# Optimization experiments

Measured on AMD Instinct MI355X. Metric: run time of the kernel, lower is better.

The kernel has to match this reference:

```python
import jax, jax.numpy as jnp
import numpy as np

N_NODES = 50000
N_EDGES = 800000
N_GRAPHS = 64
FEAT, EMB, HID, VOCAB = 128, 256, 512, 512


def setup_inputs() -> dict:
    key = jax.random.key(0)
    ks = jax.random.split(key, 16)
    def w(k, shape, fan_in):
        return jax.random.normal(k, shape, jnp.float32) / np.sqrt(fan_in)
    return {
        "prev_symbol": jax.random.randint(ks[0], (N_GRAPHS,), 0, VOCAB, jnp.int32),
        "x": jax.random.normal(ks[1], (N_NODES, FEAT), jnp.float32),
        "edge_index": jax.random.randint(ks[2], (2, N_EDGES), 0, N_NODES, jnp.int64),
        "batch": jnp.sort(jax.random.randint(ks[3], (N_NODES,), 0, N_GRAPHS, jnp.int64)),
        "W_root1": w(ks[4], (FEAT, EMB), FEAT),
        "W_rel1": w(ks[5], (FEAT, EMB), FEAT),
        "b1": jnp.zeros((EMB,), jnp.float32),
        "W_root2": w(ks[6], (EMB, HID), EMB),
        "W_rel2": w(ks[7], (EMB, HID), EMB),
        "b2": jnp.zeros((HID,), jnp.float32),
        "Wh": w(ks[8], (HID, HID), HID),
        "bh": jnp.zeros((HID,), jnp.float32),
        "Wc": w(ks[9], (HID, HID), HID),
        "bc": jnp.zeros((HID,), jnp.float32),
        "Wout": w(ks[10], (HID, VOCAB), HID),
        "bout": jnp.zeros((VOCAB,), jnp.float32),
    }


def _rgcn(x, edge_index, W_root, W_rel, b):
    # single-relation RGCNConv: root transform + mean-aggregated neighbor messages
    src, dst = edge_index[0], edge_index[1]
    msg = x[src] @ W_rel                                   # [E, out]
    agg = jax.ops.segment_sum(msg, dst, num_segments=N_NODES)
    cnt = jax.ops.segment_sum(jnp.ones((src.shape[0],), x.dtype), dst,
                              num_segments=N_NODES)
    agg = agg / jnp.maximum(cnt, 1.0)[:, None]
    return x @ W_root + agg + b


def reference(prev_symbol, x, edge_index, batch,
              W_root1, W_rel1, b1, W_root2, W_rel2, b2,
              Wh, bh, Wc, bc, Wout, bout):
    h = jax.nn.relu(_rgcn(x, edge_index, W_root1, W_rel1, b1))
    h = jax.nn.relu(_rgcn(h, edge_index, W_root2, W_rel2, b2))
    # global_mean_pool over graph ids
    s = jax.ops.segment_sum(h, batch, num_segments=N_GRAPHS)
    n = jax.ops.segment_sum(jnp.ones((h.shape[0],), h.dtype), batch,
                            num_segments=N_GRAPHS)
    pooled = s / jnp.maximum(n, 1.0)[:, None]              # [G, HID]
    hidden = pooled @ Wh + bh
    cell = pooled @ Wc + bc
    logits = jax.nn.log_softmax(hidden @ Wout + bout, axis=1)
    return (logits, hidden, cell)
```

## Files before the change

### kernel.cpp

```cpp
#include <hip/hip_runtime.h>
#include <hip/hip_bf16.h>

#define N_NODES 50000
#define N_EDGES 800000
#define N_GRAPHS 64
#define FEAT 128
#define EMB 256
#define HID 512
#define VOCAB 512

#define RB ((N_NODES + 127) / 128)
#define RPX ((RB + 7) / 8)
#define EPT 8
#define EPB (256 * EPT)
#define FILL_BLOCKS ((N_EDGES + EPB - 1) / EPB)
#define BKT 64
#define CONV_ELEMS (N_NODES * 32 + 256 * 256 + 512 * 512)
#define CONV_BLOCKS (CONV_ELEMS / 256)

typedef __attribute__((ext_vector_type(4))) float floatx4;
typedef __attribute__((ext_vector_type(2))) float floatx2;
typedef unsigned int uint32;
typedef unsigned char uchar_t;

__device__ __forceinline__ void accf8(uint32 u, float* a) {
    floatx2 lo = __builtin_amdgcn_cvt_pk_f32_fp8(u, false);
    floatx2 hi = __builtin_amdgcn_cvt_pk_f32_fp8(u, true);
    a[0] += lo[0]; a[1] += lo[1]; a[2] += hi[0]; a[3] += hi[1];
}
__device__ __forceinline__ uchar_t f2f8(float v) {
    return (uchar_t)(__builtin_amdgcn_cvt_pk_fp8_f32(v, v, 0, false) & 0xff);
}
__device__ __forceinline__ uint32 pk4f8(float a, float b, float c, float d) {
    uint32 w = __builtin_amdgcn_cvt_pk_fp8_f32(a, b, 0, false);
    return __builtin_amdgcn_cvt_pk_fp8_f32(c, d, w, true);
}
__device__ __forceinline__ void async16(const void* g, void* l) {
    __builtin_amdgcn_global_load_lds(
        (const __attribute__((address_space(1))) void*)g,
        (__attribute__((address_space(3))) void*)l, 16, 0, 0);
}

__global__ void prep_kernel(const int* __restrict__ edge, int* __restrict__ cursor,
                            int* __restrict__ srcbuf,
                            const float* __restrict__ x,
                            const float* __restrict__ W01, const float* __restrict__ W11,
                            const float* __restrict__ W02, const float* __restrict__ W12,
                            uchar_t* __restrict__ xa8,
                            uchar_t* __restrict__ w1t8, uchar_t* __restrict__ w2t8) {
    if (blockIdx.x < FILL_BLOCKS) {
        int base = blockIdx.x * EPB + threadIdx.x;
        #pragma unroll
        for (int i = 0; i < EPT; ++i) {
            int e = base + i * 256;
            if (e < N_EDGES) {
                int dst = edge[N_EDGES + e];
                int src = edge[e];
                int pos = atomicAdd(cursor + dst, 1);
                if (pos < BKT) srcbuf[(dst << 6) + pos] = src;
            }
        }
    } else {
        int tid = (blockIdx.x - FILL_BLOCKS) * 256 + threadIdx.x;
        if (tid < N_NODES * 32) {
            int row = tid >> 5, c = (tid & 31) * 4;
            float4 v = *(const float4*)(x + (size_t)row * FEAT + c);
            *(uint32*)(xa8 + (size_t)row * 256 + c) = pk4f8(v.x, v.y, v.z, v.w);
        } else if (tid < N_NODES * 32 + 256 * 256) {
            int t1 = tid - N_NODES * 32;
            int n = t1 >> 8, k = t1 & 255;
            float v = (k < 128) ? W01[(size_t)k * 256 + n] : W11[(size_t)(k - 128) * 256 + n];
            w1t8[t1] = f2f8(v);
        } else {
            int t2 = tid - N_NODES * 32 - 256 * 256;
            int n = t2 >> 9, k = t2 & 511;
            float v = (k < 256) ? W02[(size_t)k * 512 + n] : W12[(size_t)(k - 256) * 512 + n];
            w2t8[t2] = f2f8(v);
        }
    }
}

__global__ __launch_bounds__(256) void gather1_kernel(
    const int* __restrict__ cursor, const int* __restrict__ srcbuf,
    uchar_t* __restrict__ xa8)
{
    int node = blockIdx.x * 4 + (threadIdx.x >> 6);
    if (node >= N_NODES) return;
    int lane = threadIdx.x & 63;
    int grp = lane >> 3;
    int l8 = lane & 7;
    int cnt = cursor[node];
    float ri = 1.0f / (float)max(cnt, 1);
    int beg = node << 6;
    int end = beg + min(cnt, BKT);

    float a[16];
    #pragma unroll
    for (int k = 0; k < 16; ++k) a[k] = 0.f;

    int j = beg + grp;
    for (; j + 8 < end; j += 16) {
        int s0 = srcbuf[j];
        int s1 = srcbuf[j + 8];
        uint4 u0 = *(const uint4*)(xa8 + (size_t)s0 * 256 + l8 * 16);
        uint4 u1 = *(const uint4*)(xa8 + (size_t)s1 * 256 + l8 * 16);
        accf8(u0.x, a + 0); accf8(u0.y, a + 4); accf8(u0.z, a + 8); accf8(u0.w, a + 12);
        accf8(u1.x, a + 0); accf8(u1.y, a + 4); accf8(u1.z, a + 8); accf8(u1.w, a + 12);
    }
    for (; j < end; j += 8) {
        int s0 = srcbuf[j];
        uint4 u0 = *(const uint4*)(xa8 + (size_t)s0 * 256 + l8 * 16);
        accf8(u0.x, a + 0); accf8(u0.y, a + 4); accf8(u0.z, a + 8); accf8(u0.w, a + 12);
    }
    #pragma unroll
    for (int k = 0; k < 16; ++k) a[k] += __shfl_down(a[k], 32);
    #pragma unroll
    for (int k = 0; k < 16; ++k) a[k] += __shfl_down(a[k], 16);
    #pragma unroll
    for (int k = 0; k < 16; ++k) a[k] += __shfl_down(a[k], 8);
    if (grp == 0) {
        uint4 o;
        o.x = pk4f8(a[0] * ri,  a[1] * ri,  a[2] * ri,  a[3] * ri);
        o.y = pk4f8(a[4] * ri,  a[5] * ri,  a[6] * ri,  a[7] * ri);
        o.z = pk4f8(a[8] * ri,  a[9] * ri,  a[10] * ri, a[11] * ri);
        o.w = pk4f8(a[12] * ri, a[13] * ri, a[14] * ri, a[15] * ri);
        *(uint4*)(xa8 + (size_t)node * 256 + 128 + l8 * 16) = o;
    }
}

__global__ __launch_bounds__(256) void gather2_kernel(
    const int* __restrict__ cursor, const int* __restrict__ srcbuf,
    uchar_t* __restrict__ h1a8)
{
    int node = blockIdx.x * 4 + (threadIdx.x >> 6);
    if (node >= N_NODES) return;
    int lane = threadIdx.x & 63;
    int grp = lane >> 4;
    int l16 = lane & 15;
    int cnt = cursor[node];
    float ri = 1.0f / (float)max(cnt, 1);
    int beg = node << 6;
    int end = beg + min(cnt, BKT);

    float a[16];
    #pragma unroll
    for (int k = 0; k < 16; ++k) a[k] = 0.f;

    int j = beg + grp;
    for (; j + 4 < end; j += 8) {
        int s0 = srcbuf[j];
        int s1 = srcbuf[j + 4];
        uint4 u0 = *(const uint4*)(h1a8 + (size_t)s0 * 512 + l16 * 16);
        uint4 u1 = *(const uint4*)(h1a8 + (size_t)s1 * 512 + l16 * 16);
        accf8(u0.x, a + 0); accf8(u0.y, a + 4); accf8(u0.z, a + 8); accf8(u0.w, a + 12);
        accf8(u1.x, a + 0); accf8(u1.y, a + 4); accf8(u1.z, a + 8); accf8(u1.w, a + 12);
    }
    for (; j < end; j += 4) {
        int s0 = srcbuf[j];
        uint4 u0 = *(const uint4*)(h1a8 + (size_t)s0 * 512 + l16 * 16);
        accf8(u0.x, a + 0); accf8(u0.y, a + 4); accf8(u0.z, a + 8); accf8(u0.w, a + 12);
    }
    #pragma unroll
    for (int k = 0; k < 16; ++k) a[k] += __shfl_down(a[k], 32);
    #pragma unroll
    for (int k = 0; k < 16; ++k) a[k] += __shfl_down(a[k], 16);
    if (grp == 0) {
        uint4 o;
        o.x = pk4f8(a[0] * ri,  a[1] * ri,  a[2] * ri,  a[3] * ri);
        o.y = pk4f8(a[4] * ri,  a[5] * ri,  a[6] * ri,  a[7] * ri);
        o.z = pk4f8(a[8] * ri,  a[9] * ri,  a[10] * ri, a[11] * ri);
        o.w = pk4f8(a[12] * ri, a[13] * ri, a[14] * ri, a[15] * ri);
        *(uint4*)(h1a8 + (size_t)node * 512 + 256 + l16 * 16) = o;
    }
}

template<int KTOT, int OUTSTR, bool POOL, int COLS>
__global__ __launch_bounds__(256) void mfma_gemm_f8(
    const uchar_t* __restrict__ A, const uchar_t* __restrict__ Bt,
    const float* __restrict__ bias, uchar_t* __restrict__ outf8,
    float* __restrict__ psum, const int* __restrict__ batch)
{
    __shared__ uchar_t As[16384];
    __shared__ uchar_t Bs[16384];
    __shared__ float pool2[8 * 128];

    const int id = blockIdx.x;
    const int xcd = id & 7;
    const int s_ = id >> 3;
    const int col = s_ & (COLS - 1);
    const int rloc = s_ / COLS;
    const int rowblk = xcd * RPX + rloc;
    if (rowblk >= RB) return;

    const int tid = threadIdx.x;
    const int lane = tid & 63;
    const int wave = tid >> 6;
    const int quad = lane >> 4;
    const int l16 = lane & 15;
    const int m0w = (wave & 1) * 64;
    const int n0w = (wave >> 1) * 64;
    const int row0 = rowblk * 128;
    const int col0 = col * 128;
    const int Mm1 = N_NODES - 1;

    int st_r[4], st_q[4];
    #pragma unroll
    for (int c = 0; c < 4; ++c) {
        int slot = c * 256 + tid;
        int r = slot >> 3;
        st_r[c] = r;
        st_q[c] = ((slot & 7) ^ (r & 7)) * 16;
    }

    floatx4 acc[4][4] = {};

    for (int kt = 0; kt < KTOT / 128; ++kt) {
        const int kb = kt * 128;
        #pragma unroll
        for (int c = 0; c < 4; ++c) {
            async16(A + (size_t)min(row0 + st_r[c], Mm1) * KTOT + kb + st_q[c],
                    &As[(c * 256 + wave * 64) * 16]);
        }
        #pragma unroll
        for (int c = 0; c < 4; ++c) {
            async16(Bt + (size_t)(col0 + st_r[c]) * KTOT + kb + st_q[c],
                    &Bs[(c * 256 + wave * 64) * 16]);
        }
        __syncthreads();
        #pragma unroll
        for (int kk = 0; kk < 4; ++kk) {
            const int c0 = kk * 2 + (quad >> 1);
            const int o8 = (quad & 1) * 8;
            long a[4], b[4];
            #pragma unroll
            for (int t = 0; t < 4; ++t) {
                int r = m0w + t * 16 + l16;
                a[t] = *(const long*)&As[r * 128 + ((c0 ^ (r & 7)) * 16) + o8];
            }
            #pragma unroll
            for (int t = 0; t < 4; ++t) {
                int r = n0w + t * 16 + l16;
                b[t] = *(const long*)&Bs[r * 128 + ((c0 ^ (r & 7)) * 16) + o8];
            }
            #pragma unroll
            for (int i = 0; i < 4; ++i)
                #pragma unroll
                for (int j = 0; j < 4; ++j)
                    acc[i][j] = __builtin_amdgcn_mfma_f32_16x16x32_fp8_fp8(a[i], b[j], acc[i][j], 0, 0, 0);
        }
        __syncthreads();
    }

    float bias4[4];
    #pragma unroll
    for (int j = 0; j < 4; ++j) bias4[j] = bias[col0 + n0w + j * 16 + l16];

    if (!POOL) {
        #pragma unroll
        for (int i = 0; i < 4; ++i) {
            #pragma unroll
            for (int r = 0; r < 4; ++r) {
                int m = row0 + m0w + i * 16 + quad * 4 + r;
                if (m < N_NODES) {
                    #pragma unroll
                    for (int j = 0; j < 4; ++j) {
                        float v = fmaxf(acc[i][j][r] + bias4[j], 0.f);
                        outf8[(size_t)m * OUTSTR + col0 + n0w + j * 16 + l16] = f2f8(v);
                    }
                }
            }
        }
    } else {
        int gmin = batch[row0];
        int gmax = batch[min(row0 + 127, N_NODES - 1)];
        int span = gmax - gmin + 1;
        if (span == 1) {
            float s[4] = {0.f, 0.f, 0.f, 0.f};
            #pragma unroll
            for (int i = 0; i < 4; ++i) {
                #pragma unroll
                for (int r = 0; r < 4; ++r) {
                    int m = row0 + m0w + i * 16 + quad * 4 + r;
                    if (m < N_NODES) {
                        #pragma unroll
                        for (int j = 0; j < 4; ++j)
                            s[j] += fmaxf(acc[i][j][r] + bias4[j], 0.f);
                    }
                }
            }
            int slot = (wave & 1) * 4 + quad;
            #pragma unroll
            for (int j = 0; j < 4; ++j)
                pool2[slot * 128 + n0w + j * 16 + l16] = s[j];
            __syncthreads();
            if (tid < 128) {
                float v = 0.f;
                #pragma unroll
                for (int k = 0; k < 8; ++k) v += pool2[k * 128 + tid];
                atomicAdd(psum + (size_t)gmin * HID + col0 + tid, v);
            }
        } else if (span <= 8) {
            for (int i = tid; i < span * 128; i += 256) pool2[i] = 0.f;
            __syncthreads();
            float s[4] = {0.f, 0.f, 0.f, 0.f};
            int cg = -1;
            #pragma unroll
            for (int i = 0; i < 4; ++i) {
                #pragma unroll
                for (int r = 0; r < 4; ++r) {
                    int m = row0 + m0w + i * 16 + quad * 4 + r;
                    if (m < N_NODES) {
                        int g = batch[m] - gmin;
                        if (g != cg) {
                            if (cg >= 0) {
                                #pragma unroll
                                for (int j = 0; j < 4; ++j)
                                    atomicAdd(&pool2[cg * 128 + n0w + j * 16 + l16], s[j]);
                            }
                            cg = g;
                            s[0] = s[1] = s[2] = s[3] = 0.f;
                        }
                        #pragma unroll
                        for (int j = 0; j < 4; ++j)
                            s[j] += fmaxf(acc[i][j][r] + bias4[j], 0.f);
                    }
                }
            }
            if (cg >= 0) {
                #pragma unroll
                for (int j = 0; j < 4; ++j)
                    atomicAdd(&pool2[cg * 128 + n0w + j * 16 + l16], s[j]);
            }
            __syncthreads();
            for (int i = tid; i < span * 128; i += 256) {
                float v = pool2[i];
                if (v != 0.f)
                    atomicAdd(psum + (size_t)(gmin + (i >> 7)) * HID + col0 + (i & 127), v);
            }
        } else {
            #pragma unroll
            for (int i = 0; i < 4; ++i) {
                #pragma unroll
                for (int r = 0; r < 4; ++r) {
                    int m = row0 + m0w + i * 16 + quad * 4 + r;
                    if (m < N_NODES) {
                        int g = batch[m];
                        #pragma unroll
                        for (int j = 0; j < 4; ++j) {
                            float v = fmaxf(acc[i][j][r] + bias4[j], 0.f);
                            atomicAdd(psum + (size_t)g * HID + col0 + n0w + j * 16 + l16, v);
                        }
                    }
                }
            }
        }
    }
}

__global__ __launch_bounds__(64) void head_hc_kernel(
    const float* __restrict__ psum, const int* __restrict__ batch,
    const float* __restrict__ Wh, const float* __restrict__ bh,
    const float* __restrict__ Wc, const float* __restrict__ bc,
    float* __restrict__ out)
{
    __shared__ float p[HID];
    const int tile = blockIdx.x, g = blockIdx.y, t = threadIdx.x;
    #pragma unroll
    for (int i = 0; i < 8; ++i)
        p[i * 64 + t] = psum[(size_t)g * HID + i * 64 + t];
    __syncthreads();
    int col = tile * 64 + t;
    float h = 0.f, c = 0.f;
    #pragma unroll 8
    for (int k = 0; k < HID; ++k) {
        float pk = p[k];
        h += pk * Wh[(size_t)k * HID + col];
        c += pk * Wc[(size_t)k * HID + col];
    }
    int lo = 0, hi = N_NODES;
    while (lo < hi) { int mid = (lo + hi) >> 1; if (batch[mid] < g) lo = mid + 1; else hi = mid; }
    int lo2 = lo, hi2 = N_NODES;
    while (lo2 < hi2) { int mid = (lo2 + hi2) >> 1; if (batch[mid] < g + 1) lo2 = mid + 1; else hi2 = mid; }
    float inv = 1.0f / fmaxf((float)(lo2 - lo), 1.0f);
    out[(size_t)N_GRAPHS * VOCAB + (size_t)g * HID + col] = fmaf(h, inv, bh[col]);
    out[(size_t)2 * N_GRAPHS * VOCAB + (size_t)g * HID + col] = fmaf(c, inv, bc[col]);
}

__global__ __launch_bounds__(512) void head_out_kernel(
    const float* __restrict__ hidden, const float* __restrict__ Wout,
    const float* __restrict__ bout, float* __restrict__ out)
{
    __shared__ float hrow[HID];
    __shared__ float redm[8];
    __shared__ float reds[8];
    __shared__ float bm, bs;
    const int g = blockIdx.x, j = threadIdx.x;
    hrow[j] = hidden[(size_t)g * HID + j];
    __syncthreads();
    float l = bout[j];
    #pragma unroll 8
    for (int k = 0; k < HID; ++k)
        l += hrow[k] * Wout[(size_t)k * VOCAB + j];

    const int lane = j & 63, wave = j >> 6;
    float m = l;
    #pragma unroll
    for (int o = 32; o > 0; o >>= 1) m = fmaxf(m, __shfl_down(m, o));
    if (lane == 0) redm[wave] = m;
    __syncthreads();
    if (j == 0) {
        float mm = redm[0];
        for (int w = 1; w < 8; ++w) mm = fmaxf(mm, redm[w]);
        bm = mm;
    }
    __syncthreads();
    m = bm;
    float e = __expf(l - m);
    float s = e;
    #pragma unroll
    for (int o = 32; o > 0; o >>= 1) s += __shfl_down(s, o);
    if (lane == 0) reds[wave] = s;
    __syncthreads();
    if (j == 0) {
        float ss = 0.f;
        for (int w = 0; w < 8; ++w) ss += reds[w];
        bs = ss;
    }
    __syncthreads();
    out[(size_t)g * VOCAB + j] = l - m - logf(bs);
}

extern "C" void kernel_launch(void* const* d_in, const int* in_sizes, int n_in,
                              void* d_out, int out_size, void* d_ws, size_t ws_size,
                              hipStream_t stream) {
    const float* x      = (const float*)d_in[1];
    const int*   edge   = (const int*)d_in[2];
    const int*   batch  = (const int*)d_in[3];
    const float* Wroot1 = (const float*)d_in[4];
    const float* Wrel1  = (const float*)d_in[5];
    const float* b1     = (const float*)d_in[6];
    const float* Wroot2 = (const float*)d_in[7];
    const float* Wrel2  = (const float*)d_in[8];
    const float* b2     = (const float*)d_in[9];
    const float* Wh     = (const float*)d_in[10];
    const float* bh     = (const float*)d_in[11];
    const float* Wc     = (const float*)d_in[12];
    const float* bc     = (const float*)d_in[13];
    const float* Wout   = (const float*)d_in[14];
    const float* bout   = (const float*)d_in[15];
    float* out = (float*)d_out;

    int*      cursor  = (int*)d_ws;
    float*    psum    = (float*)(cursor + N_NODES);
    int*      srcbuf  = (int*)(psum + N_GRAPHS * HID);
    uchar_t*  xa8     = (uchar_t*)(srcbuf + (size_t)N_NODES * BKT);
    uchar_t*  w1t8    = xa8 + (size_t)N_NODES * 256;
    uchar_t*  h1a8    = w1t8 + 256 * 256;
    uchar_t*  w2t8    = h1a8 + (size_t)N_NODES * 512;

    hipMemsetAsync(d_ws, 0, (size_t)(N_NODES + N_GRAPHS * HID) * 4, stream);

    prep_kernel<<<FILL_BLOCKS + CONV_BLOCKS, 256, 0, stream>>>(
        edge, cursor, srcbuf, x, Wroot1, Wrel1, Wroot2, Wrel2, xa8, w1t8, w2t8);

    gather1_kernel<<<(N_NODES + 3) / 4, 256, 0, stream>>>(cursor, srcbuf, xa8);

    {
        mfma_gemm_f8<256, 512, false, 2><<<8 * RPX * 2, 256, 0, stream>>>(
            xa8, w1t8, b1, h1a8, nullptr, nullptr);
    }

    gather2_kernel<<<(N_NODES + 3) / 4, 256, 0, stream>>>(cursor, srcbuf, h1a8);

    {
        mfma_gemm_f8<512, 0, true, 4><<<8 * RPX * 4, 256, 0, stream>>>(
            h1a8, w2t8, b2, nullptr, psum, batch);
    }

    head_hc_kernel<<<dim3(8, 64), 64, 0, stream>>>(psum, batch, Wh, bh, Wc, bc, out);
    head_out_kernel<<<N_GRAPHS, 512, 0, stream>>>(
        out + (size_t)N_GRAPHS * VOCAB, Wout, bout, out);
}
```

Before: 321.8 us.

## Replace global per-node atomics with two-pass bucketed edge binning

Edge-to-CSR binning now runs in two passes. The first pass does a block-local histogram into 98 buckets of 512 nodes each, reserves space with one global atomic per bucket, and writes (src,dst) pairs into coarse bucket buffers. A new bucket kernel then uses LDS atomics to place sources into per-node slots and write counts. This removes 800K contended global atomics and scattered writes, at the cost of an extra kernel launch, an intermediate buffer, and a fixed bucket capacity that silently drops edges if a bucket overflows.

```diff
diff --git a/kernel.cpp b/kernel.cpp
--- a/kernel.cpp
+++ b/kernel.cpp
@@ -11,10 +11,14 @@
 
 #define RB ((N_NODES + 127) / 128)
 #define RPX ((RB + 7) / 8)
-#define EPT 8
-#define EPB (256 * EPT)
-#define FILL_BLOCKS ((N_EDGES + EPB - 1) / EPB)
 #define BKT 64
+
+#define NPB 98
+#define BCAP 10240
+#define PA_EDGES 4096
+#define PA_BLOCKS ((N_EDGES + PA_EDGES - 1) / PA_EDGES)
+#define BC_STR 16
+
 #define CONV_ELEMS (N_NODES * 32 + 256 * 256 + 512 * 512)
 #define CONV_BLOCKS (CONV_ELEMS / 256)
 
@@ -41,27 +45,56 @@
         (__attribute__((address_space(3))) void*)l, 16, 0, 0);
 }
 
-__global__ void prep_kernel(const int* __restrict__ edge, int* __restrict__ cursor,
-                            int* __restrict__ srcbuf,
+__global__ void prep_kernel(const int* __restrict__ edge, int* __restrict__ bktcnt,
+                            int2* __restrict__ bktbuf,
                             const float* __restrict__ x,
                             const float* __restrict__ W01, const float* __restrict__ W11,
                             const float* __restrict__ W02, const float* __restrict__ W12,
                             uchar_t* __restrict__ xa8,
                             uchar_t* __restrict__ w1t8, uchar_t* __restrict__ w2t8) {
-    if (blockIdx.x < FILL_BLOCKS) {
-        int base = blockIdx.x * EPB + threadIdx.x;
-        #pragma unroll
-        for (int i = 0; i < EPT; ++i) {
-            int e = base + i * 256;
-            if (e < N_EDGES) {
-                int dst = edge[N_EDGES + e];
-                int src = edge[e];
-                int pos = atomicAdd(cursor + dst, 1);
-                if (pos < BKT) srcbuf[(dst << 6) + pos] = src;
-            }
+    if (blockIdx.x < PA_BLOCKS) {
+        __shared__ int hist[NPB];
+        __shared__ int excl[NPB];
+        __shared__ int lpos[NPB];
+        __shared__ int gbase[NPB];
+        __shared__ int2 stage[PA_EDGES];
+        const int t = threadIdx.x;
+        const int e0 = blockIdx.x * PA_EDGES;
+        const int ne = min(PA_EDGES, N_EDGES - e0);
+
+        if (t < NPB) hist[t] = 0;
+        __syncthreads();
+        for (int s = t; s < ne; s += 256) {
+            int d = edge[N_EDGES + e0 + s];
+            atomicAdd(&hist[d >> 9], 1);
+        }
+        __syncthreads();
+        if (t == 0) {
+            int run = 0;
+            for (int i = 0; i < NPB; ++i) { excl[i] = run; run += hist[i]; }
+        }
+        __syncthreads();
+        if (t < NPB) {
+            gbase[t] = atomicAdd(bktcnt + t * BC_STR, hist[t]);
+            lpos[t] = excl[t];
+        }
+        __syncthreads();
+        for (int s = t; s < ne; s += 256) {
+            int src = edge[e0 + s];
+            int d = edge[N_EDGES + e0 + s];
+            int b = d >> 9;
+            int lp = atomicAdd(&lpos[b], 1);
+            stage[lp] = make_int2(src, d);
+        }
+        __syncthreads();
+        for (int s = t; s < ne; s += 256) {
+            int2 p = stage[s];
+            int b = p.y >> 9;
+            int g = gbase[b] + (s - excl[b]);
+            if (g < BCAP) bktbuf[(size_t)b * BCAP + g] = p;
         }
     } else {
-        int tid = (blockIdx.x - FILL_BLOCKS) * 256 + threadIdx.x;
+        int tid = (blockIdx.x - PA_BLOCKS) * 256 + threadIdx.x;
         if (tid < N_NODES * 32) {
             int row = tid >> 5, c = (tid & 31) * 4;
             float4 v = *(const float4*)(x + (size_t)row * FEAT + c);
@@ -80,8 +113,34 @@
     }
 }
 
+__global__ __launch_bounds__(256) void bucket_kernel(const int* __restrict__ bktcnt,
+                                                     const int2* __restrict__ bktbuf,
+                                                     int* __restrict__ srcbuf,
+                                                     int* __restrict__ cnt) {
+    __shared__ int lcur[512];
+    const int b = blockIdx.x;
+    const int t = threadIdx.x;
+    const int n0 = b << 9;
+    const int nn = min(512, N_NODES - n0);
+    const int ne = min(bktcnt[b * BC_STR], BCAP);
+
+    #pragma unroll
+    for (int i = t; i < 512; i += 256) lcur[i] = 0;
+    __syncthreads();
+    for (int s = t; s < ne; s += 256) {
+        int2 p = bktbuf[(size_t)b * BCAP + s];
+        int d = p.y & 511;
+        int k = atomicAdd(&lcur[d], 1);
+        if (k < BKT) srcbuf[((size_t)(n0 + d) << 6) + k] = p.x;
+    }
+    __syncthreads();
+    #pragma unroll
+    for (int i = t; i < 512; i += 256)
+        if (i < nn) cnt[n0 + i] = lcur[i];
+}
+
 __global__ __launch_bounds__(256) void gather1_kernel(
-    const int* __restrict__ cursor, const int* __restrict__ srcbuf,
+    const int* __restrict__ cnt, const int* __restrict__ srcbuf,
     uchar_t* __restrict__ xa8)
 {
     int node = blockIdx.x * 4 + (threadIdx.x >> 6);
@@ -89,10 +148,10 @@
     int lane = threadIdx.x & 63;
     int grp = lane >> 3;
     int l8 = lane & 7;
-    int cnt = cursor[node];
-    float ri = 1.0f / (float)max(cnt, 1);
+    int c_ = cnt[node];
+    float ri = 1.0f / (float)max(c_, 1);
     int beg = node << 6;
-    int end = beg + min(cnt, BKT);
+    int end = beg + min(c_, BKT);
 
     float a[16];
     #pragma unroll
@@ -129,7 +188,7 @@
 }
 
 __global__ __launch_bounds__(256) void gather2_kernel(
-    const int* __restrict__ cursor, const int* __restrict__ srcbuf,
+    const int* __restrict__ cnt, const int* __restrict__ srcbuf,
     uchar_t* __restrict__ h1a8)
 {
     int node = blockIdx.x * 4 + (threadIdx.x >> 6);
@@ -137,10 +196,10 @@
     int lane = threadIdx.x & 63;
     int grp = lane >> 4;
     int l16 = lane & 15;
-    int cnt = cursor[node];
-    float ri = 1.0f / (float)max(cnt, 1);
+    int c_ = cnt[node];
+    float ri = 1.0f / (float)max(c_, 1);
     int beg = node << 6;
-    int end = beg + min(cnt, BKT);
+    int end = beg + min(c_, BKT);
 
     float a[16];
     #pragma unroll
@@ -450,27 +509,31 @@
     const float* bout   = (const float*)d_in[15];
     float* out = (float*)d_out;
 
-    int*      cursor  = (int*)d_ws;
-    float*    psum    = (float*)(cursor + N_NODES);
-    int*      srcbuf  = (int*)(psum + N_GRAPHS * HID);
-    uchar_t*  xa8     = (uchar_t*)(srcbuf + (size_t)N_NODES * BKT);
+    int*      bktcnt  = (int*)d_ws;
+    float*    psum    = (float*)(bktcnt + 128 * BC_STR);
+    int*      cnt     = (int*)(psum + N_GRAPHS * HID);
+    int*      srcbuf  = cnt + N_NODES;
+    int2*     bktbuf  = (int2*)(srcbuf + (size_t)N_NODES * BKT);
+    uchar_t*  xa8     = (uchar_t*)(bktbuf + (size_t)NPB * BCAP);
     uchar_t*  w1t8    = xa8 + (size_t)N_NODES * 256;
     uchar_t*  h1a8    = w1t8 + 256 * 256;
     uchar_t*  w2t8    = h1a8 + (size_t)N_NODES * 512;
 
-    hipMemsetAsync(d_ws, 0, (size_t)(N_NODES + N_GRAPHS * HID) * 4, stream);
-
-    prep_kernel<<<FILL_BLOCKS + CONV_BLOCKS, 256, 0, stream>>>(
-        edge, cursor, srcbuf, x, Wroot1, Wrel1, Wroot2, Wrel2, xa8, w1t8, w2t8);
-
-    gather1_kernel<<<(N_NODES + 3) / 4, 256, 0, stream>>>(cursor, srcbuf, xa8);
+    hipMemsetAsync(d_ws, 0, (size_t)(128 * BC_STR + N_GRAPHS * HID) * 4, stream);
+
+    prep_kernel<<<PA_BLOCKS + CONV_BLOCKS, 256, 0, stream>>>(
+        edge, bktcnt, bktbuf, x, Wroot1, Wrel1, Wroot2, Wrel2, xa8, w1t8, w2t8);
+
+    bucket_kernel<<<NPB, 256, 0, stream>>>(bktcnt, bktbuf, srcbuf, cnt);
+
+    gather1_kernel<<<(N_NODES + 3) / 4, 256, 0, stream>>>(cnt, srcbuf, xa8);
 
     {
         mfma_gemm_f8<256, 512, false, 2><<<8 * RPX * 2, 256, 0, stream>>>(
             xa8, w1t8, b1, h1a8, nullptr, nullptr);
     }
 
-    gather2_kernel<<<(N_NODES + 3) / 4, 256, 0, stream>>>(cursor, srcbuf, h1a8);
+    gather2_kernel<<<(N_NODES + 3) / 4, 256, 0, stream>>>(cnt, srcbuf, h1a8);
 
     {
         mfma_gemm_f8<512, 0, true, 4><<<8 * RPX * 4, 256, 0, stream>>>(
```

Result: faster. 311.9 us (-3.1%).
